# Kernel optimization log

Measured on AMD Instinct MI355X. Metric: run time of the kernel, lower is better.

The kernel has to match this reference:

```python
import jax, jax.numpy as jnp
import numpy as np

N_USERS = 50000
N_ITEMS = 75000
N_NODES = N_USERS + N_ITEMS
NNZ = 1250000
EMB = 64
N_LAYERS = 3
BATCH = 4096
EPS = 1e-12


def setup_inputs() -> dict:
    key = jax.random.key(0)
    ks = jax.random.split(key, 12)
    xavier = float(np.sqrt(6.0 / (EMB + EMB)))
    return {
        "user": jax.random.randint(ks[0], (BATCH,), 0, N_USERS, dtype=jnp.int64 if jax.config.jax_enable_x64 else jnp.int32),
        "pos_item": jax.random.randint(ks[1], (BATCH,), 0, N_ITEMS, dtype=jnp.int32),
        "neg_item": jax.random.randint(ks[2], (BATCH,), 0, N_ITEMS, dtype=jnp.int32),
        "row": jax.random.randint(ks[3], (NNZ,), 0, N_NODES, dtype=jnp.int32),
        "col": jax.random.randint(ks[4], (NNZ,), 0, N_NODES, dtype=jnp.int32),
        "vals": jax.random.uniform(ks[5], (NNZ,), dtype=jnp.float32),
        "emb": jax.random.normal(ks[6], (N_NODES, EMB), dtype=jnp.float32) * 0.1,
        "W1": jax.random.uniform(ks[7], (N_LAYERS, EMB, EMB), minval=-xavier, maxval=xavier, dtype=jnp.float32),
        "b1": jnp.zeros((N_LAYERS, EMB), dtype=jnp.float32),
        "W2": jax.random.uniform(ks[8], (N_LAYERS, EMB, EMB), minval=-xavier, maxval=xavier, dtype=jnp.float32),
        "b2": jnp.zeros((N_LAYERS, EMB), dtype=jnp.float32),
    }


def _l2_normalize(x):
    n = jnp.linalg.norm(x, axis=-1, keepdims=True)
    return x / jnp.maximum(n, EPS)


def reference(user, pos_item, neg_item, row, col, vals, emb, W1, b1, W2, b2):
    # eval mode: node_dropout / mess_dropout inactive (rates 0)
    node_feat = emb
    all_embeddings = [node_feat]
    for l in range(N_LAYERS):
        # sparse SpMM: agg[i] = sum_j A[i,j] * node_feat[j]
        msg = vals[:, None] * node_feat[col]            # [nnz, d]
        agg = jax.ops.segment_sum(msg, row, num_segments=N_NODES)  # [N, d]
        part_1 = jax.nn.leaky_relu(agg @ W1[l].T + b1[l], 0.2)
        part_2 = jax.nn.leaky_relu((agg * node_feat) @ W2[l].T + b2[l], 0.2)
        node_feat = part_1 + part_2
        all_embeddings.append(_l2_normalize(node_feat))
    embedding_weight = jnp.concatenate(all_embeddings, axis=-1)  # [N, 4*d]
    gcn_user = embedding_weight[:N_USERS]
    gcn_item = embedding_weight[N_USERS:]
    return (gcn_user[user], gcn_item[pos_item], gcn_item[neg_item])
```

## Files before the change

kernel.cpp:

```cpp
#include <hip/hip_runtime.h>
#include <hip/hip_fp16.h>

#define N_USERS 50000
#define N_ITEMS 75000
#define N_NODES 125000
#define N_PAD   125008
#define NNZ     1250000
#define EMB     64
#define N_LAYERS 3
#define BATCH   4096
#define CONCAT  256

#define BROWS   128
#define NB      ((N_NODES + BROWS - 1) / BROWS)
#define CHUNK   4096
#define NCHUNK  ((NNZ + CHUNK - 1) / CHUNK)
#define EPT     (CHUNK / 256)
#define BCAP    1600
#define FB_NODES 64
#define NBLK    ((N_NODES + FB_NODES - 1) / FB_NODES)
#define SCAP    8

#define F4      (N_NODES * EMB / 4)
#define G4      (3 * BATCH * EMB / 4)
#define SM      (3 * BATCH)
#define INIT_ITEMS (F4 + G4 + SM)
#define INIT_BLOCKS ((INIT_ITEMS + 255) / 256)

typedef _Float16 half8  __attribute__((ext_vector_type(8)));
typedef _Float16 half4  __attribute__((ext_vector_type(4)));
typedef float    floatx4 __attribute__((ext_vector_type(4)));

__device__ __forceinline__ bool user_is_i64(const void* uptr) {
    const int* u = (const int*)uptr;
    return (u[1] | u[3] | u[5] | u[7]) == 0;
}
__device__ __forceinline__ int load_user(const void* uptr, int b, bool is64) {
    return is64 ? (int)((const long long*)uptr)[b] : ((const int*)uptr)[b];
}
__device__ __forceinline__ int sample_node(const void* user, const int* pos,
                                           const int* neg, int which, int b,
                                           bool is64) {
    if (which == 0) return load_user(user, b, is64);
    return N_USERS + (which == 1 ? pos[b] : neg[b]);
}

__device__ __forceinline__ float unpack_val(unsigned w) {
    unsigned short us = (unsigned short)(w >> 17);
    _Float16 h = __builtin_bit_cast(_Float16, us);
    return (float)h;
}

__global__ __launch_bounds__(256) void part_init_kernel(
    const int* __restrict__ row, const int* __restrict__ col,
    const float* __restrict__ vals, const float* __restrict__ emb,
    const void* __restrict__ user, const int* __restrict__ pos,
    const int* __restrict__ neg,
    _Float16* __restrict__ f16, float* __restrict__ out,
    int* __restrict__ bcnt, int* __restrict__ scnt, int* __restrict__ smap,
    unsigned long long* __restrict__ sw8) {

    __shared__ int h[NB];
    __shared__ int base[NB];

    if (blockIdx.x < NCHUNK) {
        int t = threadIdx.x;
        int e0 = blockIdx.x * CHUNK;
        int e1 = e0 + CHUNK; if (e1 > NNZ) e1 = NNZ;
        for (int i = t; i < NB; i += 256) h[i] = 0;
        __syncthreads();

        unsigned long long rec[EPT];
        int bkt[EPT];
        int ps[EPT];
        int cnt = 0;
        for (int e = e0 + t; e < e1; e += 256) {
            int r = row[e];
            int b = r >> 7;
            _Float16 hv = (_Float16)vals[e];
            unsigned hb = (unsigned)__builtin_bit_cast(unsigned short, hv);
            rec[cnt] = ((unsigned long long)hb << 24)
                     | ((unsigned)(r & 127) << 17)
                     | (unsigned)col[e];
            bkt[cnt] = b;
            ps[cnt] = atomicAdd(&h[b], 1);
            ++cnt;
        }
        __syncthreads();
        for (int i = t; i < NB; i += 256) {
            int c = h[i];
            if (c) base[i] = atomicAdd(&bcnt[i], c);
        }
        __syncthreads();
        for (int k = 0; k < cnt; ++k) {
            int b = bkt[k];
            sw8[(size_t)b * BCAP + base[b] + ps[k]] = rec[k];
        }
    } else {
        int idx = (blockIdx.x - NCHUNK) * 256 + threadIdx.x;
        bool is64 = user_is_i64(user);
        if (idx < F4) {
            floatx4 v = *(const floatx4*)(emb + (size_t)idx * 4);
            half4 o;
            #pragma unroll
            for (int i = 0; i < 4; ++i) o[i] = (_Float16)v[i];
            *(half4*)(f16 + (size_t)idx * 4) = o;
        } else if (idx < F4 + G4) {
            int j = idx - F4;
            int which = j / (BATCH * 16);
            int rem   = j % (BATCH * 16);
            int bb = rem >> 4, c4 = rem & 15;
            int node = sample_node(user, pos, neg, which, bb, is64);
            floatx4 v = *(const floatx4*)(emb + (size_t)node * EMB + c4 * 4);
            *(floatx4*)(out + (size_t)(which * BATCH + bb) * CONCAT + c4 * 4) = v;
        } else if (idx < F4 + G4 + SM) {
            int g2 = idx - F4 - G4;
            int which = g2 / BATCH, bb = g2 % BATCH;
            int node = sample_node(user, pos, neg, which, bb, is64);
            int slot = atomicAdd(&scnt[node], 1);
            if (slot < SCAP) smap[node * SCAP + slot] = g2;
        }
    }
}

__global__ __launch_bounds__(256) void bucket_sort_kernel(
    const int* __restrict__ bcnt,
    const unsigned long long* __restrict__ sw8,
    unsigned* __restrict__ se, int* __restrict__ off, int* __restrict__ endv) {
    __shared__ unsigned long long ew[BCAP];
    __shared__ unsigned eo[BCAP];
    __shared__ int rh[BROWS], rb[BROWS], rc[BROWS];
    __shared__ int s[256];

    int b = blockIdx.x, t = threadIdx.x;
    int n = bcnt[b];
    int s0 = b * BCAP;
    if (t < BROWS) rh[t] = 0;
    __syncthreads();
    const unsigned long long* src = sw8 + (size_t)b * BCAP;
    for (int i = t; i < n; i += 256) {
        unsigned long long rec = src[i];
        ew[i] = rec;
        atomicAdd(&rh[(int)((rec >> 17) & 127)], 1);
    }
    __syncthreads();
    s[t] = (t < BROWS) ? rh[t] : 0;
    __syncthreads();
    for (int d = 1; d < 256; d <<= 1) {
        int x = (t >= d) ? s[t - d] : 0;
        __syncthreads();
        s[t] += x;
        __syncthreads();
    }
    if (t < BROWS) {
        int excl = s[t] - rh[t];
        rb[t] = excl;
        rc[t] = 0;
        int r = b * BROWS + t;
        if (r < N_NODES) {
            off[r]  = s0 + excl;
            endv[r] = s0 + s[t];
        }
    }
    __syncthreads();
    for (int i = t; i < n; i += 256) {
        unsigned long long rec = ew[i];
        int r = (int)((rec >> 17) & 127);
        int p = rb[r] + atomicAdd(&rc[r], 1);
        eo[p] = (unsigned)(((rec >> 24) << 17) | (rec & 0x1FFFFULL));
    }
    __syncthreads();
    for (int i = t; i < n; i += 256)
        se[(size_t)s0 + i] = eo[i];
}

__global__ __launch_bounds__(256) void layer_kernel(
    const int* __restrict__ off, const int* __restrict__ endv,
    const unsigned* __restrict__ se,
    const _Float16* __restrict__ fin, _Float16* __restrict__ fout,
    const float* __restrict__ W1, const float* __restrict__ b1,
    const float* __restrict__ W2, const float* __restrict__ b2,
    const int* __restrict__ scnt, const int* __restrict__ smap,
    float* __restrict__ out, int layer) {

    __shared__ _Float16 wlds[2][EMB][EMB];
    __shared__ _Float16 alds[FB_NODES][EMB];

    int tid = threadIdx.x;

    {
        const float* Wsrc0 = W1 + layer * EMB * EMB;
        const float* Wsrc1 = W2 + layer * EMB * EMB;
        #pragma unroll
        for (int m = 0; m < 2; ++m) {
            const float* Ws = m ? Wsrc1 : Wsrc0;
            for (int c = tid; c < 512; c += 256) {
                int n = c >> 3, c16 = c & 7;
                const float* p = Ws + n * EMB + c16 * 8;
                floatx4 wa = *(const floatx4*)p, wb = *(const floatx4*)(p + 4);
                half8 h;
                #pragma unroll
                for (int i = 0; i < 4; ++i) {
                    h[i] = (_Float16)wa[i]; h[4 + i] = (_Float16)wb[i];
                }
                *(half8*)(&wlds[m][n][(c16 ^ (n & 7)) * 8]) = h;
            }
        }
    }

    int wave = tid >> 6, lane = tid & 63;
    int g = lane >> 3;
    int k = lane & 7;
    int base = blockIdx.x * FB_NODES;
    const _Float16* fink = fin + k * 8;

    for (int p = 0; p < 2; ++p) {
        int ln = p * 32 + wave * 8 + g;
        int node = base + ln;
        bool valid = node < N_NODES;
        int j   = valid ? off[node]  : 0;
        int end = valid ? endv[node] : 0;

        float acc[8] = {0.f, 0.f, 0.f, 0.f, 0.f, 0.f, 0.f, 0.f};
        unsigned ev[8];
        #pragma unroll
        for (int t = 0; t < 8; ++t)
            ev[t] = (j + t < end) ? se[j + t] : 0u;

        while (__any(j < end)) {
            int jn = j + 8;
            half8 h[8];
            #pragma unroll
            for (int t = 0; t < 8; ++t) {
                int c = (int)(ev[t] & 0x1FFFFu);
                h[t] = *(const half8*)(fink + (size_t)c * EMB);
            }
            unsigned evn[8];
            #pragma unroll
            for (int t = 0; t < 8; ++t)
                evn[t] = (jn + t < end) ? se[jn + t] : 0u;
            #pragma unroll
            for (int t = 0; t < 8; ++t) {
                float val = unpack_val(ev[t]);
                #pragma unroll
                for (int i = 0; i < 8; ++i)
                    acc[i] += (float)h[t][i] * val;
                ev[t] = evn[t];
            }
            j = jn;
        }
        half8 o;
        #pragma unroll
        for (int i = 0; i < 8; ++i) o[i] = (_Float16)acc[i];
        *(half8*)(&alds[ln][(k ^ (ln & 7)) * 8]) = o;
    }
    __syncthreads();

    {
        int lm = lane & 15, quad = lane >> 4;
        int ln0 = wave * 16 + lm;
        int nb = base + wave * 16;
        int nodeD = nb + lm;
        int sw = lm & 7;

        half8 a0 = *(const half8*)(&alds[ln0][(quad ^ sw) * 8]);
        half8 a1 = *(const half8*)(&alds[ln0][((quad + 4) ^ sw) * 8]);

        int nsafe = nodeD < N_NODES ? nodeD : 0;
        const half8* fp = (const half8*)(fin + (size_t)nsafe * EMB + quad * 8);
        half8 f0 = fp[0], f1 = fp[4];
        half8 g0 = a0 * f0, g1 = a1 * f1;

        float nfv[4][4];
        float sq[4] = {0.f, 0.f, 0.f, 0.f};

        #pragma unroll
        for (int t = 0; t < 4; ++t) {
            int n = t * 16 + lm;
            float bias1 = b1[layer * EMB + n];
            float bias2 = b2[layer * EMB + n];
            half8 w10 = *(const half8*)(&wlds[0][n][(quad ^ sw) * 8]);
            half8 w11 = *(const half8*)(&wlds[0][n][((quad + 4) ^ sw) * 8]);
            half8 w20 = *(const half8*)(&wlds[1][n][(quad ^ sw) * 8]);
            half8 w21 = *(const half8*)(&wlds[1][n][((quad + 4) ^ sw) * 8]);
            floatx4 d1 = {0.f, 0.f, 0.f, 0.f}, d2 = {0.f, 0.f, 0.f, 0.f};
            d1 = __builtin_amdgcn_mfma_f32_16x16x32_f16(a0, w10, d1, 0, 0, 0);
            d1 = __builtin_amdgcn_mfma_f32_16x16x32_f16(a1, w11, d1, 0, 0, 0);
            d2 = __builtin_amdgcn_mfma_f32_16x16x32_f16(g0, w20, d2, 0, 0, 0);
            d2 = __builtin_amdgcn_mfma_f32_16x16x32_f16(g1, w21, d2, 0, 0, 0);
            #pragma unroll
            for (int r = 0; r < 4; ++r) {
                float p1v = d1[r] + bias1;
                p1v = p1v > 0.f ? p1v : 0.2f * p1v;
                float p2v = d2[r] + bias2;
                p2v = p2v > 0.f ? p2v : 0.2f * p2v;
                float nf = p1v + p2v;
                nfv[t][r] = nf;
                sq[r] += nf * nf;
            }
        }

        if (layer != N_LAYERS - 1) {
            #pragma unroll
            for (int t = 0; t < 4; ++t) {
                int dim = t * 16 + lm;
                #pragma unroll
                for (int r = 0; r < 4; ++r) {
                    int nodeO = nb + quad * 4 + r;
                    if (nodeO < N_NODES)
                        fout[(size_t)nodeO * EMB + dim] = (_Float16)nfv[t][r];
                }
            }
        }

        #pragma unroll
        for (int r = 0; r < 4; ++r) {
            float v = sq[r];
            #pragma unroll
            for (int m = 1; m < 16; m <<= 1) v += __shfl_xor(v, m, 64);
            sq[r] = fmaxf(sqrtf(v), 1e-12f);
        }

        #pragma unroll
        for (int r = 0; r < 4; ++r) {
            int nodeO = nb + quad * 4 + r;
            if (nodeO >= N_NODES) continue;
            int c = scnt[nodeO]; c = c < SCAP ? c : SCAP;
            float inv = 1.0f / sq[r];
            for (int i2 = 0; i2 < c; ++i2) {
                int smp = smap[nodeO * SCAP + i2];
                float* po = out + (size_t)smp * CONCAT + (layer + 1) * EMB;
                #pragma unroll
                for (int t = 0; t < 4; ++t)
                    po[t * 16 + lm] = nfv[t][r] * inv;
            }
        }
    }
}

extern "C" void kernel_launch(void* const* d_in, const int* in_sizes, int n_in,
                              void* d_out, int out_size, void* d_ws, size_t ws_size,
                              hipStream_t stream) {
    const void* user = d_in[0];
    const int* pos  = (const int*)d_in[1];
    const int* neg  = (const int*)d_in[2];
    const int* row  = (const int*)d_in[3];
    const int* col  = (const int*)d_in[4];
    const float* vals = (const float*)d_in[5];
    const float* emb  = (const float*)d_in[6];
    const float* W1   = (const float*)d_in[7];
    const float* b1   = (const float*)d_in[8];
    const float* W2   = (const float*)d_in[9];
    const float* b2   = (const float*)d_in[10];

    _Float16* f16a   = (_Float16*)d_ws;
    _Float16* f16b   = f16a + (size_t)N_PAD * EMB;
    int*      off    = (int*)(f16b + (size_t)N_PAD * EMB);
    int*      endv   = off + (N_NODES + 8);
    int*      bcnt   = endv + (N_NODES + 8);
    int*      scnt   = bcnt + 984;
    int*      smap   = scnt + N_NODES;
    unsigned long long* sw8 = (unsigned long long*)(smap + N_NODES * SCAP);
    unsigned* se     = (unsigned*)(sw8 + (size_t)NB * BCAP);

    float* out = (float*)d_out;

    hipMemsetAsync(bcnt, 0, (size_t)(984 + N_NODES) * sizeof(int), stream);

    part_init_kernel<<<NCHUNK + INIT_BLOCKS, 256, 0, stream>>>(
        row, col, vals, emb, user, pos, neg, f16a, out, bcnt, scnt, smap, sw8);

    bucket_sort_kernel<<<NB, 256, 0, stream>>>(bcnt, sw8, se, off, endv);

    const _Float16* fin = f16a;
    _Float16* fout = f16b;
    for (int l = 0; l < N_LAYERS; ++l) {
        layer_kernel<<<NBLK, 256, 0, stream>>>(
            off, endv, se, fin, fout, W1, b1, W2, b2, scnt, smap, out, l);
        const _Float16* tmp = fout; fout = (_Float16*)fin; fin = (const _Float16*)tmp;
    }
}
```

Measured before the change: 240.6 us.

## Compute final GCN layer only for sampled batch nodes

```diff
diff --git a/kernel.cpp b/kernel.cpp
--- a/kernel.cpp
+++ b/kernel.cpp
@@ -20,6 +20,7 @@
 #define FB_NODES 64
 #define NBLK    ((N_NODES + FB_NODES - 1) / FB_NODES)
 #define SCAP    8
+#define NACT_BLK ((3 * BATCH + FB_NODES - 1) / FB_NODES)
 
 #define F4      (N_NODES * EMB / 4)
 #define G4      (3 * BATCH * EMB / 4)
@@ -58,6 +59,7 @@
     const int* __restrict__ neg,
     _Float16* __restrict__ f16, float* __restrict__ out,
     int* __restrict__ bcnt, int* __restrict__ scnt, int* __restrict__ smap,
+    int* __restrict__ nact, int* __restrict__ active,
     unsigned long long* __restrict__ sw8) {
 
     __shared__ int h[NB];
@@ -119,6 +121,10 @@
             int node = sample_node(user, pos, neg, which, bb, is64);
             int slot = atomicAdd(&scnt[node], 1);
             if (slot < SCAP) smap[node * SCAP + slot] = g2;
+            if (slot == 0) {
+                int p = atomicAdd(nact, 1);
+                active[p] = node;
+            }
         }
     }
 }
@@ -300,16 +306,14 @@
             }
         }
 
-        if (layer != N_LAYERS - 1) {
-            #pragma unroll
-            for (int t = 0; t < 4; ++t) {
-                int dim = t * 16 + lm;
-                #pragma unroll
-                for (int r = 0; r < 4; ++r) {
-                    int nodeO = nb + quad * 4 + r;
-                    if (nodeO < N_NODES)
-                        fout[(size_t)nodeO * EMB + dim] = (_Float16)nfv[t][r];
-                }
+        #pragma unroll
+        for (int t = 0; t < 4; ++t) {
+            int dim = t * 16 + lm;
+            #pragma unroll
+            for (int r = 0; r < 4; ++r) {
+                int nodeO = nb + quad * 4 + r;
+                if (nodeO < N_NODES)
+                    fout[(size_t)nodeO * EMB + dim] = (_Float16)nfv[t][r];
             }
         }
 
@@ -329,6 +333,164 @@
             float inv = 1.0f / sq[r];
             for (int i2 = 0; i2 < c; ++i2) {
                 int smp = smap[nodeO * SCAP + i2];
+                float* po = out + (size_t)smp * CONCAT + (layer + 1) * EMB;
+                #pragma unroll
+                for (int t = 0; t < 4; ++t)
+                    po[t * 16 + lm] = nfv[t][r] * inv;
+            }
+        }
+    }
+}
+
+__global__ __launch_bounds__(256) void layerL_kernel(
+    const int* __restrict__ off, const int* __restrict__ endv,
+    const unsigned* __restrict__ se,
+    const int* __restrict__ nactp, const int* __restrict__ active,
+    const _Float16* __restrict__ fin,
+    const float* __restrict__ W1, const float* __restrict__ b1,
+    const float* __restrict__ W2, const float* __restrict__ b2,
+    const int* __restrict__ scnt, const int* __restrict__ smap,
+    float* __restrict__ out, int layer) {
+
+    __shared__ _Float16 wlds[2][EMB][EMB];
+    __shared__ _Float16 alds[FB_NODES][EMB];
+
+    int tid = threadIdx.x;
+    int nact = *nactp;
+
+    {
+        const float* Wsrc0 = W1 + layer * EMB * EMB;
+        const float* Wsrc1 = W2 + layer * EMB * EMB;
+        #pragma unroll
+        for (int m = 0; m < 2; ++m) {
+            const float* Ws = m ? Wsrc1 : Wsrc0;
+            for (int c = tid; c < 512; c += 256) {
+                int n = c >> 3, c16 = c & 7;
+                const float* p = Ws + n * EMB + c16 * 8;
+                floatx4 wa = *(const floatx4*)p, wb = *(const floatx4*)(p + 4);
+                half8 h;
+                #pragma unroll
+                for (int i = 0; i < 4; ++i) {
+                    h[i] = (_Float16)wa[i]; h[4 + i] = (_Float16)wb[i];
+                }
+                *(half8*)(&wlds[m][n][(c16 ^ (n & 7)) * 8]) = h;
+            }
+        }
+    }
+
+    int wave = tid >> 6, lane = tid & 63;
+    int g = lane >> 3;
+    int k = lane & 7;
+    int base = blockIdx.x * FB_NODES;
+    const _Float16* fink = fin + k * 8;
+
+    for (int p = 0; p < 2; ++p) {
+        int ln = p * 32 + wave * 8 + g;
+        int idx = base + ln;
+        bool valid = idx < nact;
+        int node = valid ? active[idx] : 0;
+        int j   = valid ? off[node]  : 0;
+        int end = valid ? endv[node] : 0;
+
+        float acc[8] = {0.f, 0.f, 0.f, 0.f, 0.f, 0.f, 0.f, 0.f};
+        unsigned ev[8];
+        #pragma unroll
+        for (int t = 0; t < 8; ++t)
+            ev[t] = (j + t < end) ? se[j + t] : 0u;
+
+        while (__any(j < end)) {
+            int jn = j + 8;
+            half8 h[8];
+            #pragma unroll
+            for (int t = 0; t < 8; ++t) {
+                int c = (int)(ev[t] & 0x1FFFFu);
+                h[t] = *(const half8*)(fink + (size_t)c * EMB);
+            }
+            unsigned evn[8];
+            #pragma unroll
+            for (int t = 0; t < 8; ++t)
+                evn[t] = (jn + t < end) ? se[jn + t] : 0u;
+            #pragma unroll
+            for (int t = 0; t < 8; ++t) {
+                float val = unpack_val(ev[t]);
+                #pragma unroll
+                for (int i = 0; i < 8; ++i)
+                    acc[i] += (float)h[t][i] * val;
+                ev[t] = evn[t];
+            }
+            j = jn;
+        }
+        half8 o;
+        #pragma unroll
+        for (int i = 0; i < 8; ++i) o[i] = (_Float16)acc[i];
+        *(half8*)(&alds[ln][(k ^ (ln & 7)) * 8]) = o;
+    }
+    __syncthreads();
+
+    {
+        int lm = lane & 15, quad = lane >> 4;
+        int ln0 = wave * 16 + lm;
+        int idxD = base + ln0;
+        int nodeD = (idxD < nact) ? active[idxD] : -1;
+        int sw = lm & 7;
+
+        half8 a0 = *(const half8*)(&alds[ln0][(quad ^ sw) * 8]);
+        half8 a1 = *(const half8*)(&alds[ln0][((quad + 4) ^ sw) * 8]);
+
+        int nsafe = nodeD >= 0 ? nodeD : 0;
+        const half8* fp = (const half8*)(fin + (size_t)nsafe * EMB + quad * 8);
+        half8 f0 = fp[0], f1 = fp[4];
+        half8 g0 = a0 * f0, g1 = a1 * f1;
+
+        float nfv[4][4];
+        float sq[4] = {0.f, 0.f, 0.f, 0.f};
+
+        #pragma unroll
+        for (int t = 0; t < 4; ++t) {
+            int n = t * 16 + lm;
+            float bias1 = b1[layer * EMB + n];
+            float bias2 = b2[layer * EMB + n];
+            half8 w10 = *(const half8*)(&wlds[0][n][(quad ^ sw) * 8]);
+            half8 w11 = *(const half8*)(&wlds[0][n][((quad + 4) ^ sw) * 8]);
+            half8 w20 = *(const half8*)(&wlds[1][n][(quad ^ sw) * 8]);
+            half8 w21 = *(const half8*)(&wlds[1][n][((quad + 4) ^ sw) * 8]);
+            floatx4 d1 = {0.f, 0.f, 0.f, 0.f}, d2 = {0.f, 0.f, 0.f, 0.f};
+            d1 = __builtin_amdgcn_mfma_f32_16x16x32_f16(a0, w10, d1, 0, 0, 0);
+            d1 = __builtin_amdgcn_mfma_f32_16x16x32_f16(a1, w11, d1, 0, 0, 0);
+            d2 = __builtin_amdgcn_mfma_f32_16x16x32_f16(g0, w20, d2, 0, 0, 0);
+            d2 = __builtin_amdgcn_mfma_f32_16x16x32_f16(g1, w21, d2, 0, 0, 0);
+            #pragma unroll
+            for (int r = 0; r < 4; ++r) {
+                float p1v = d1[r] + bias1;
+                p1v = p1v > 0.f ? p1v : 0.2f * p1v;
+                float p2v = d2[r] + bias2;
+                p2v = p2v > 0.f ? p2v : 0.2f * p2v;
+                float nf = p1v + p2v;
+                nfv[t][r] = nf;
+                sq[r] += nf * nf;
+            }
+        }
+
+        int nodeO[4];
+        #pragma unroll
+        for (int r = 0; r < 4; ++r)
+            nodeO[r] = __shfl(nodeD, quad * 4 + r, 64);
+
+        #pragma unroll
+        for (int r = 0; r < 4; ++r) {
+            float v = sq[r];
+            #pragma unroll
+            for (int m = 1; m < 16; m <<= 1) v += __shfl_xor(v, m, 64);
+            sq[r] = fmaxf(sqrtf(v), 1e-12f);
+        }
+
+        #pragma unroll
+        for (int r = 0; r < 4; ++r) {
+            if (nodeO[r] < 0) continue;
+            int c = scnt[nodeO[r]]; c = c < SCAP ? c : SCAP;
+            float inv = 1.0f / sq[r];
+            for (int i2 = 0; i2 < c; ++i2) {
+                int smp = smap[nodeO[r] * SCAP + i2];
                 float* po = out + (size_t)smp * CONCAT + (layer + 1) * EMB;
                 #pragma unroll
                 for (int t = 0; t < 4; ++t)
@@ -359,24 +521,30 @@
     int*      endv   = off + (N_NODES + 8);
     int*      bcnt   = endv + (N_NODES + 8);
     int*      scnt   = bcnt + 984;
-    int*      smap   = scnt + N_NODES;
+    int*      nact   = scnt + N_NODES;
+    int*      active = nact + 8;
+    int*      smap   = active + 3 * BATCH;
     unsigned long long* sw8 = (unsigned long long*)(smap + N_NODES * SCAP);
     unsigned* se     = (unsigned*)(sw8 + (size_t)NB * BCAP);
 
     float* out = (float*)d_out;
 
-    hipMemsetAsync(bcnt, 0, (size_t)(984 + N_NODES) * sizeof(int), stream);
+    hipMemsetAsync(bcnt, 0, (size_t)(984 + N_NODES + 8) * sizeof(int), stream);
 
     part_init_kernel<<<NCHUNK + INIT_BLOCKS, 256, 0, stream>>>(
-        row, col, vals, emb, user, pos, neg, f16a, out, bcnt, scnt, smap, sw8);
+        row, col, vals, emb, user, pos, neg, f16a, out, bcnt, scnt, smap,
+        nact, active, sw8);
 
     bucket_sort_kernel<<<NB, 256, 0, stream>>>(bcnt, sw8, se, off, endv);
 
     const _Float16* fin = f16a;
     _Float16* fout = f16b;
-    for (int l = 0; l < N_LAYERS; ++l) {
+    for (int l = 0; l < N_LAYERS - 1; ++l) {
         layer_kernel<<<NBLK, 256, 0, stream>>>(
             off, endv, se, fin, fout, W1, b1, W2, b2, scnt, smap, out, l);
         const _Float16* tmp = fout; fout = (_Float16*)fin; fin = (const _Float16*)tmp;
     }
-}
+    layerL_kernel<<<NACT_BLK, 256, 0, stream>>>(
+        off, endv, se, nact, active, fin, W1, b1, W2, b2, scnt, smap, out,
+        N_LAYERS - 1);
+}
```

Result: faster. 230.1 us (median of 2 runs) (-4.4%).
